# Optimization experiments

Measured on AMD Instinct MI355X. Metric: run time of the kernel, lower is better.

Reference implementation:

```python
import math
import jax, jax.numpy as jnp
import numpy as np

# Module hyperparameters (match init_kwargs)
EMBED = 512
H = 8            # n_heads
D = EMBED // H   # head_dim = 64
P = 32           # poly_dim
M = 4            # num_prf_features
R = 1            # num_quadrature_nodes
B = 1
T = 1024
EPS = 1e-6
C_CONST = 2.0 + EPS
# Gauss-Laguerre nodes/weights (R=1 -> node=1, weight=1), scaled by 1/C as in __init__
_nodes_np, _weights_np = np.polynomial.laguerre.laggauss(R)
QUAD_NODES = (_nodes_np / C_CONST).astype(np.float32)   # [R]


def setup_inputs() -> dict:
    key = jax.random.key(0)
    ks = jax.random.split(key, 6)
    x = jax.random.normal(ks[0], (B, T, EMBED), dtype=jnp.float32)
    qkv_w = jax.random.normal(ks[1], (3 * EMBED, EMBED), dtype=jnp.float32) * 0.02
    qkv_b = jnp.zeros((3 * EMBED,), dtype=jnp.float32)
    out_w = jax.random.normal(ks[2], (EMBED, EMBED), dtype=jnp.float32) * 0.02
    out_b = jnp.zeros((EMBED,), dtype=jnp.float32)
    omega = jax.random.normal(ks[3], (R, H, D, M), dtype=jnp.float32)  # PRF projection buffer
    poly_proj = jax.random.normal(ks[4], (H, D, P), dtype=jnp.float32) / math.sqrt(D)
    return {"x": x, "qkv_w": qkv_w, "qkv_b": qkv_b, "out_w": out_w,
            "out_b": out_b, "omega": omega, "poly_proj": poly_proj}


def _l2_normalize(z):
    # F.normalize(p=2, dim=-1), default eps=1e-12
    n = jnp.linalg.norm(z, axis=-1, keepdims=True)
    return z / jnp.maximum(n, 1e-12)


def _prf_features(x_norm, omega):
    # x_norm: [B,H,T,D], omega: [R,H,D,M] -> [R,B,H,T,M]
    proj = jnp.einsum('bhtd,rhdm->rbhtm', x_norm, omega)
    s = jnp.asarray(QUAD_NODES, x_norm.dtype).reshape(R, 1, 1, 1, 1)
    sqrt_2s = jnp.sqrt(2.0 * jnp.maximum(s, 0.0))
    exp_arg = jnp.clip(proj * sqrt_2s - s, -20.0, 20.0)
    return jnp.exp(exp_arg) / math.sqrt(M)


def _poly_features(x_norm, poly_proj):
    # squared random projection: [B,H,T,D] x [H,D,P] -> [B,H,T,P], nonneg
    p = jnp.einsum('bhtd,hdp->bhtp', x_norm, poly_proj)
    return p * p


def reference(x, qkv_w, qkv_b, out_w, out_b, omega, poly_proj):
    Bx, Tx, Cx = x.shape
    qkv = x @ qkv_w.T + qkv_b                       # [B,T,3C]
    q, k, v = jnp.split(qkv, 3, axis=-1)
    def to_heads(z):
        return z.reshape(Bx, Tx, H, D).transpose(0, 2, 1, 3)  # [B,H,T,D]
    q, k, v = to_heads(q), to_heads(k), to_heads(v)

    def full_features(z):
        zn = _l2_normalize(z)
        poly = _poly_features(zn, poly_proj)        # [B,H,T,P]
        prf = _prf_features(zn, omega)              # [R,B,H,T,M]
        return jnp.einsum('bhtp,rbhtm->rbhtpm', poly, prf)

    q_outer = full_features(q)                      # [R,B,H,T,P,M]
    k_outer = full_features(k)

    kv = jnp.einsum('rbhtpm,bhtd->rbhtpmd', k_outer, v)  # huge outer product
    kv_cumsum = jnp.cumsum(kv, axis=3)              # causal prefix sums along T
    k_cumsum = jnp.cumsum(k_outer, axis=3)

    context = jnp.einsum('rbhtpm,rbhtpmd->bhtd', q_outer, kv_cumsum)
    norm = jnp.einsum('rbhtpm,rbhtpm->bht', q_outer, k_cumsum)
    norm = jnp.maximum(norm, 1e-6)
    out = context / norm[..., None]                 # [B,H,T,D]

    out = out.transpose(0, 2, 1, 3).reshape(Bx, Tx, Cx)
    return out @ out_w.T + out_b
```

## Files before the change

kernel.cpp:

```cpp
#include <hip/hip_runtime.h>

#define T_LEN 1024
#define EMB   512
#define NH    8
#define HD    64
#define PDIM  32
#define MDIM  4
#define FDIM  128
#define TC    64
#define NC    16

typedef __attribute__((ext_vector_type(8))) short bf16x8;
typedef __attribute__((ext_vector_type(4))) float f32x4;

__device__ __forceinline__ unsigned short f2bf(float f) {
    unsigned u = __float_as_uint(f);
    unsigned r = u + 0x7fffu + ((u >> 16) & 1u);
    return (unsigned short)(r >> 16);
}
__device__ __forceinline__ float bf2f(unsigned short h) {
    return __uint_as_float(((unsigned)h) << 16);
}
__device__ __forceinline__ void split4(float4 v, ushort4& h4, ushort4& l4) {
    h4.x = f2bf(v.x); l4.x = f2bf(v.x - bf2f(h4.x));
    h4.y = f2bf(v.y); l4.y = f2bf(v.y - bf2f(h4.y));
    h4.z = f2bf(v.z); l4.z = f2bf(v.z - bf2f(h4.z));
    h4.w = f2bf(v.w); l4.w = f2bf(v.w - bf2f(h4.w));
}
__device__ __forceinline__ f32x4 mm3(bf16x8 ah, bf16x8 al, bf16x8 bh, bf16x8 bl, f32x4 acc) {
    acc = __builtin_amdgcn_mfma_f32_16x16x32_bf16(ah, bh, acc, 0, 0, 0);
    acc = __builtin_amdgcn_mfma_f32_16x16x32_bf16(ah, bl, acc, 0, 0, 0);
    acc = __builtin_amdgcn_mfma_f32_16x16x32_bf16(al, bh, acc, 0, 0, 0);
    return acc;
}
#define LD8(TILE, ROW, KB) (*reinterpret_cast<const bf16x8*>(&TILE[ROW][KB]))

__global__ __launch_bounds__(256) void k_cvt(
    const float* __restrict__ X, const float* __restrict__ Wq,
    const float* __restrict__ Wo,
    unsigned short* __restrict__ Xhi, unsigned short* __restrict__ Xlo,
    unsigned short* __restrict__ Whi, unsigned short* __restrict__ Wlo,
    unsigned short* __restrict__ Ohi, unsigned short* __restrict__ Olo)
{
    int i = (blockIdx.x * 256 + threadIdx.x) * 4;
    const float* src; unsigned short *dh, *dl; int off;
    if (i < 524288)       { src = X;  dh = Xhi; dl = Xlo; off = i; }
    else if (i < 1310720) { src = Wq; dh = Whi; dl = Wlo; off = i - 524288; }
    else                  { src = Wo; dh = Ohi; dl = Olo; off = i - 1310720; }
    float4 v = *reinterpret_cast<const float4*>(&src[off]);
    ushort4 h4, l4; split4(v, h4, l4);
    *reinterpret_cast<ushort4*>(&dh[off]) = h4;
    *reinterpret_cast<ushort4*>(&dl[off]) = l4;
}

__global__ __launch_bounds__(256) void k_qkv_mfma(
    const unsigned short* __restrict__ Xhi, const unsigned short* __restrict__ Xlo,
    const unsigned short* __restrict__ Whi, const unsigned short* __restrict__ Wlo,
    const float* __restrict__ bias,
    const float* __restrict__ poly_proj, const float* __restrict__ omega,
    unsigned short* __restrict__ Vhi, unsigned short* __restrict__ Vlo,
    unsigned short* __restrict__ qfhi, unsigned short* __restrict__ qflo,
    unsigned short* __restrict__ kfhi, unsigned short* __restrict__ kflo)
{
    const int j0 = blockIdx.x * 64;
    const int t0 = blockIdx.y * 64;
    __shared__ __align__(16) unsigned short Ahi[64][80], Alo[64][80],
                                            Bhi[64][80], Blo[64][80];
    __shared__ float poly_s[64][33];
    __shared__ float prf_s[64][5];
    __shared__ float nrm2[2][64];
    const int tid = threadIdx.x, lane = tid & 63, wid = tid >> 6;
    const int wrow = (wid >> 1) * 32, wcol = (wid & 1) * 32;
    const int lr = lane & 15, lg = lane >> 4;
    f32x4 acc[2][2];
    #pragma unroll
    for (int i = 0; i < 2; ++i)
        #pragma unroll
        for (int j = 0; j < 2; ++j) acc[i][j] = (f32x4){0.f, 0.f, 0.f, 0.f};

    for (int k0 = 0; k0 < 512; k0 += 64) {
        #pragma unroll
        for (int l = 0; l < 2; ++l) {
            int ch = tid + l * 256;
            int row = ch >> 3, sg = (ch & 7) * 8;
            size_t ao = (size_t)(t0 + row) * 512 + k0 + sg;
            size_t bo = (size_t)(j0 + row) * 512 + k0 + sg;
            *reinterpret_cast<int4*>(&Ahi[row][sg]) = *reinterpret_cast<const int4*>(&Xhi[ao]);
            *reinterpret_cast<int4*>(&Alo[row][sg]) = *reinterpret_cast<const int4*>(&Xlo[ao]);
            *reinterpret_cast<int4*>(&Bhi[row][sg]) = *reinterpret_cast<const int4*>(&Whi[bo]);
            *reinterpret_cast<int4*>(&Blo[row][sg]) = *reinterpret_cast<const int4*>(&Wlo[bo]);
        }
        __syncthreads();
        #pragma unroll
        for (int kh = 0; kh < 2; ++kh) {
            const int kb = kh * 32 + lg * 8;
            bf16x8 ah0 = LD8(Ahi, wrow + lr, kb),      ah1 = LD8(Ahi, wrow + 16 + lr, kb);
            bf16x8 al0 = LD8(Alo, wrow + lr, kb),      al1 = LD8(Alo, wrow + 16 + lr, kb);
            bf16x8 bh0 = LD8(Bhi, wcol + lr, kb),      bh1 = LD8(Bhi, wcol + 16 + lr, kb);
            bf16x8 bl0 = LD8(Blo, wcol + lr, kb),      bl1 = LD8(Blo, wcol + 16 + lr, kb);
            acc[0][0] = mm3(ah0, al0, bh0, bl0, acc[0][0]);
            acc[0][1] = mm3(ah0, al0, bh1, bl1, acc[0][1]);
            acc[1][0] = mm3(ah1, al1, bh0, bl0, acc[1][0]);
            acc[1][1] = mm3(ah1, al1, bh1, bl1, acc[1][1]);
        }
        __syncthreads();
    }
    const int which = j0 >> 9;
    const int h = (j0 & 511) >> 6;

    if (which == 2) {
        #pragma unroll
        for (int i = 0; i < 2; ++i)
            #pragma unroll
            for (int j = 0; j < 2; ++j)
                #pragma unroll
                for (int r = 0; r < 4; ++r) {
                    int row = wrow + i * 16 + lg * 4 + r;
                    int col = wcol + j * 16 + lr;
                    float val = acc[i][j][r] + bias[j0 + col];
                    unsigned short hv = f2bf(val);
                    size_t vi = (size_t)(h * T_LEN + t0 + row) * HD + col;
                    Vhi[vi] = hv; Vlo[vi] = f2bf(val - bf2f(hv));
                }
        return;
    }

    #pragma unroll
    for (int i = 0; i < 2; ++i) {
        #pragma unroll
        for (int r = 0; r < 4; ++r) {
            int row = wrow + i * 16 + lg * 4 + r;
            float ss = 0.f;
            #pragma unroll
            for (int j = 0; j < 2; ++j) {
                int col = wcol + j * 16 + lr;
                float zv = acc[i][j][r] + bias[j0 + col];
                ss = fmaf(zv, zv, ss);
                unsigned short hv = f2bf(zv);
                Ahi[row][col] = hv;
                Alo[row][col] = f2bf(zv - bf2f(hv));
            }
            ss += __shfl_xor(ss, 1, 64);
            ss += __shfl_xor(ss, 2, 64);
            ss += __shfl_xor(ss, 4, 64);
            ss += __shfl_xor(ss, 8, 64);
            if (lr == 0) nrm2[wid & 1][row] = ss;
        }
    }
    {
        const float* P = poly_proj + (size_t)h * 64 * 32;
        int d = tid >> 2, p8 = (tid & 3) * 8;
        #pragma unroll
        for (int e = 0; e < 8; ++e) {
            float pv = P[d * 32 + p8 + e];
            unsigned short hv = f2bf(pv);
            Bhi[p8 + e][d] = hv;
            Blo[p8 + e][d] = f2bf(pv - bf2f(hv));
        }
        if (tid < 64) {
            const float* Om = omega + (size_t)h * 64 * 4;
            float4 om = *reinterpret_cast<const float4*>(&Om[tid * 4]);
            float oa[4] = {om.x, om.y, om.z, om.w};
            #pragma unroll
            for (int m = 0; m < 4; ++m) {
                unsigned short hv = f2bf(oa[m]);
                Bhi[32 + m][tid] = hv;
                Blo[32 + m][tid] = f2bf(oa[m] - bf2f(hv));
            }
        }
        for (int rr = tid; rr < 12 * 64; rr += 256) {
            int row = 36 + (rr >> 6), dd = rr & 63;
            Bhi[row][dd] = 0; Blo[row][dd] = 0;
        }
    }
    __syncthreads();
    const int mrow = wid * 16;
    f32x4 g[3];
    g[0] = g[1] = g[2] = (f32x4){0.f, 0.f, 0.f, 0.f};
    #pragma unroll
    for (int kh = 0; kh < 2; ++kh) {
        const int kb = kh * 32 + lg * 8;
        bf16x8 ah = LD8(Ahi, mrow + lr, kb), al = LD8(Alo, mrow + lr, kb);
        #pragma unroll
        for (int j = 0; j < 3; ++j) {
            bf16x8 bh = LD8(Bhi, j * 16 + lr, kb), bl = LD8(Blo, j * 16 + lr, kb);
            g[j] = mm3(ah, al, bh, bl, g[j]);
        }
    }
    const float S_NODE = (float)(1.0 / 2.000001);
    const float SQRT2S = sqrtf(2.0f * S_NODE);
    #pragma unroll
    for (int r = 0; r < 4; ++r) {
        int row = mrow + lg * 4 + r;
        float rn = 1.0f / fmaxf(sqrtf(nrm2[0][row] + nrm2[1][row]), 1e-12f);
        #pragma unroll
        for (int j = 0; j < 3; ++j) {
            float gv = g[j][r] * rn;
            if (j < 2) poly_s[row][j * 16 + lr] = gv * gv;
            else if (lr < 4) {
                float arg = fminf(fmaxf(fmaf(gv, SQRT2S, -S_NODE), -20.0f), 20.0f);
                prf_s[row][lr] = expf(arg) * 0.5f;
            }
        }
    }
    {
        int row = mrow + (lane >> 2), fq = lane & 3;
        float pr[8], pf[4];
        #pragma unroll
        for (int e = 0; e < 8; ++e) pr[e] = poly_s[row][fq * 8 + e];
        #pragma unroll
        for (int m = 0; m < 4; ++m) pf[m] = prf_s[row][m];
        int4 hi4[4], lo4[4];
        unsigned short* hp = reinterpret_cast<unsigned short*>(hi4);
        unsigned short* lp = reinterpret_cast<unsigned short*>(lo4);
        #pragma unroll
        for (int e = 0; e < 8; ++e)
            #pragma unroll
            for (int m = 0; m < 4; ++m) {
                float val = pr[e] * pf[m];
                unsigned short hv = f2bf(val);
                hp[e * 4 + m] = hv;
                lp[e * 4 + m] = f2bf(val - bf2f(hv));
            }
        unsigned short* dhi = (which == 0) ? qfhi : kfhi;
        unsigned short* dlo = (which == 0) ? qflo : kflo;
        size_t base = (size_t)(h * T_LEN + t0 + row) * FDIM + fq * 32;
        #pragma unroll
        for (int s = 0; s < 4; ++s) {
            *reinterpret_cast<int4*>(&dhi[base + s * 8]) = hi4[s];
            *reinterpret_cast<int4*>(&dlo[base + s * 8]) = lo4[s];
        }
    }
}

__global__ __launch_bounds__(256) void k_out_mfma(
    const unsigned short* __restrict__ AThi, const unsigned short* __restrict__ ATlo,
    const unsigned short* __restrict__ Ohi, const unsigned short* __restrict__ Olo,
    const float* __restrict__ bias, float* __restrict__ Y)
{
    const int j0 = blockIdx.x * 64;
    const int t0 = blockIdx.y * 64;
    __shared__ __align__(16) unsigned short Ahi[64][80], Alo[64][80],
                                            Bhi[64][80], Blo[64][80];
    const int tid = threadIdx.x, lane = tid & 63, wid = tid >> 6;
    const int wrow = (wid >> 1) * 32, wcol = (wid & 1) * 32;
    const int lr = lane & 15, lg = lane >> 4;
    f32x4 acc[2][2];
    #pragma unroll
    for (int i = 0; i < 2; ++i)
        #pragma unroll
        for (int j = 0; j < 2; ++j) acc[i][j] = (f32x4){0.f, 0.f, 0.f, 0.f};

    for (int k0 = 0; k0 < 512; k0 += 64) {
        #pragma unroll
        for (int l = 0; l < 2; ++l) {
            int ch = tid + l * 256;
            int row = ch >> 3, sg = (ch & 7) * 8;
            size_t ao = (size_t)(t0 + row) * 512 + k0 + sg;
            size_t bo = (size_t)(j0 + row) * 512 + k0 + sg;
            *reinterpret_cast<int4*>(&Ahi[row][sg]) = *reinterpret_cast<const int4*>(&AThi[ao]);
            *reinterpret_cast<int4*>(&Alo[row][sg]) = *reinterpret_cast<const int4*>(&ATlo[ao]);
            *reinterpret_cast<int4*>(&Bhi[row][sg]) = *reinterpret_cast<const int4*>(&Ohi[bo]);
            *reinterpret_cast<int4*>(&Blo[row][sg]) = *reinterpret_cast<const int4*>(&Olo[bo]);
        }
        __syncthreads();
        #pragma unroll
        for (int kh = 0; kh < 2; ++kh) {
            const int kb = kh * 32 + lg * 8;
            bf16x8 ah0 = LD8(Ahi, wrow + lr, kb),      ah1 = LD8(Ahi, wrow + 16 + lr, kb);
            bf16x8 al0 = LD8(Alo, wrow + lr, kb),      al1 = LD8(Alo, wrow + 16 + lr, kb);
            bf16x8 bh0 = LD8(Bhi, wcol + lr, kb),      bh1 = LD8(Bhi, wcol + 16 + lr, kb);
            bf16x8 bl0 = LD8(Blo, wcol + lr, kb),      bl1 = LD8(Blo, wcol + 16 + lr, kb);
            acc[0][0] = mm3(ah0, al0, bh0, bl0, acc[0][0]);
            acc[0][1] = mm3(ah0, al0, bh1, bl1, acc[0][1]);
            acc[1][0] = mm3(ah1, al1, bh0, bl0, acc[1][0]);
            acc[1][1] = mm3(ah1, al1, bh1, bl1, acc[1][1]);
        }
        __syncthreads();
    }
    #pragma unroll
    for (int i = 0; i < 2; ++i)
        #pragma unroll
        for (int j = 0; j < 2; ++j)
            #pragma unroll
            for (int r = 0; r < 4; ++r) {
                int row = wrow + i * 16 + lg * 4 + r;
                int col = wcol + j * 16 + lr;
                Y[(size_t)(t0 + row) * EMB + j0 + col] = acc[i][j][r] + bias[j0 + col];
            }
}

__global__ __launch_bounds__(256) void k_chunk_kv(
    const unsigned short* __restrict__ kfhi, const unsigned short* __restrict__ kflo,
    const unsigned short* __restrict__ Vhi, const unsigned short* __restrict__ Vlo,
    float* __restrict__ SchT, float* __restrict__ zch,
    unsigned short* __restrict__ Vthi, unsigned short* __restrict__ Vtlo)
{
    const int b = blockIdx.x;
    const int fh = b & 1, hc = b >> 1, h = hc >> 4, c = hc & 15;
    const int t0 = c * TC;
    const int tid = threadIdx.x, lane = tid & 63, wid = tid >> 6;
    const int wrow = (wid >> 1) * 32, wcol = (wid & 1) * 32;
    const int lr = lane & 15, lg = lane >> 4;
    __shared__ __align__(16) unsigned short Khi[64][80], Klo[64][80],
                                            Ghi[64][80], Glo[64][80];
    #pragma unroll
    for (int l = 0; l < 2; ++l) {
        int ch = tid + l * 256;
        int t = ch >> 3, f8 = (ch & 7) * 8;
        int tb = t >> 3, tl = t & 7, m = f8 >> 3;
        size_t ko = (size_t)((h << 10) + t0 + t) * FDIM + fh * 64 + f8;
        int4 hv = *reinterpret_cast<const int4*>(&kfhi[ko]);
        int4 lv = *reinterpret_cast<const int4*>(&kflo[ko]);
        const unsigned short* hp = reinterpret_cast<const unsigned short*>(&hv);
        const unsigned short* lp = reinterpret_cast<const unsigned short*>(&lv);
        int col = ((tb ^ m) << 3) + tl;
        #pragma unroll
        for (int j = 0; j < 8; ++j) {
            Khi[f8 + j][col] = hp[j];
            Klo[f8 + j][col] = lp[j];
        }
    }
    #pragma unroll
    for (int l = 0; l < 4; ++l) {
        int ch = tid + l * 256;
        int plane = ch >> 9, rem = ch & 511;
        int t = rem >> 3, d8 = (rem & 7) * 8;
        int tb = t >> 3, tl = t & 7;
        const unsigned short* src = plane ? Vlo : Vhi;
        int4 vv = *reinterpret_cast<const int4*>(&src[(size_t)((h << 10) + t0 + t) * HD + d8]);
        const unsigned short* vp = reinterpret_cast<const unsigned short*>(&vv);
        int col = ((tb ^ (d8 >> 3)) << 3) + tl;
        unsigned short (*dst)[80] = plane ? Glo : Ghi;
        #pragma unroll
        for (int j = 0; j < 8; ++j) dst[d8 + j][col] = vp[j];
    }
    __syncthreads();
    f32x4 acc[2][2];
    #pragma unroll
    for (int i = 0; i < 2; ++i)
        #pragma unroll
        for (int j = 0; j < 2; ++j) acc[i][j] = (f32x4){0.f, 0.f, 0.f, 0.f};
    #pragma unroll
    for (int kh = 0; kh < 2; ++kh) {
        const int kb = kh * 32 + lg * 8, cb = kb >> 3;
        const int f0r = wcol + lr, f1r = wcol + 16 + lr;
        const int c0 = ((cb ^ ((f0r >> 3) & 7)) << 3), c1 = ((cb ^ ((f1r >> 3) & 7)) << 3);
        bf16x8 bh0 = *reinterpret_cast<const bf16x8*>(&Khi[f0r][c0]);
        bf16x8 bl0 = *reinterpret_cast<const bf16x8*>(&Klo[f0r][c0]);
        bf16x8 bh1 = *reinterpret_cast<const bf16x8*>(&Khi[f1r][c1]);
        bf16x8 bl1 = *reinterpret_cast<const bf16x8*>(&Klo[f1r][c1]);
        #pragma unroll
        for (int di = 0; di < 2; ++di) {
            int dr = wrow + di * 16 + lr;
            int ca = ((cb ^ ((dr >> 3) & 7)) << 3);
            bf16x8 ah = *reinterpret_cast<const bf16x8*>(&Ghi[dr][ca]);
            bf16x8 al = *reinterpret_cast<const bf16x8*>(&Glo[dr][ca]);
            acc[di][0] = mm3(ah, al, bh0, bl0, acc[di][0]);
            acc[di][1] = mm3(ah, al, bh1, bl1, acc[di][1]);
        }
    }
    if (tid < 64) {
        float s = 0.f;
        const int g = (tid >> 3) & 7;
        #pragma unroll
        for (int cb2 = 0; cb2 < 8; ++cb2) {
            int base = ((cb2 ^ g) << 3);
            #pragma unroll
            for (int e = 0; e < 8; ++e)
                s += bf2f(Khi[tid][base + e]) + bf2f(Klo[tid][base + e]);
        }
        zch[(h * NC + c) * FDIM + fh * 64 + tid] = s;
    }
    if (fh == 0) {
        #pragma unroll
        for (int l = 0; l < 4; ++l) {
            int ch = tid + l * 256;
            int plane = ch >> 9, rem = ch & 511;
            int d = rem >> 3, m = rem & 7;
            int g = (d >> 3) & 7;
            const unsigned short (*src)[80] = plane ? Glo : Ghi;
            unsigned short* dst = plane ? Vtlo : Vthi;
            *reinterpret_cast<int4*>(&dst[(size_t)(h * HD + d) * T_LEN + t0 + ((m ^ g) << 3)]) =
                *reinterpret_cast<const int4*>(&src[d][m << 3]);
        }
    }
    float* S = SchT + (size_t)(h * NC + c) * FDIM * HD;
    #pragma unroll
    for (int di = 0; di < 2; ++di)
        #pragma unroll
        for (int fj = 0; fj < 2; ++fj)
            #pragma unroll
            for (int r = 0; r < 4; ++r) {
                int d = wrow + di * 16 + lg * 4 + r;
                int f = fh * 64 + wcol + fj * 16 + lr;
                S[d * FDIM + f] = acc[di][fj][r];
            }
}

__global__ __launch_bounds__(256) void k_prefix(
    const float* __restrict__ SchT, const float* __restrict__ zch,
    unsigned short* __restrict__ SThi, unsigned short* __restrict__ STlo,
    float* __restrict__ zpre)
{
    const int h = blockIdx.x >> 4;
    const int e = ((blockIdx.x & 15) << 9) + threadIdx.x * 2;
    const size_t base = (size_t)h * NC * FDIM * HD + e;
    float2 vals[NC];
    #pragma unroll
    for (int c = 0; c < NC; ++c)
        vals[c] = *reinterpret_cast<const float2*>(&SchT[base + (size_t)c * FDIM * HD]);
    float r0 = 0.f, r1 = 0.f;
    #pragma unroll
    for (int c = 0; c < NC; ++c) {
        unsigned short h0 = f2bf(r0), h1 = f2bf(r1);
        unsigned short l0 = f2bf(r0 - bf2f(h0)), l1 = f2bf(r1 - bf2f(h1));
        size_t wi = base + (size_t)c * FDIM * HD;
        *reinterpret_cast<unsigned*>(&SThi[wi]) = (unsigned)h0 | ((unsigned)h1 << 16);
        *reinterpret_cast<unsigned*>(&STlo[wi]) = (unsigned)l0 | ((unsigned)l1 << 16);
        r0 += vals[c].x; r1 += vals[c].y;
    }
    if ((blockIdx.x & 15) == 0 && threadIdx.x < FDIM) {
        const int zb = h * NC * FDIM + threadIdx.x;
        float zv[NC];
        #pragma unroll
        for (int c = 0; c < NC; ++c) zv[c] = zch[zb + c * FDIM];
        float zr = 0.0f;
        #pragma unroll
        for (int c = 0; c < NC; ++c) { zpre[zb + c * FDIM] = zr; zr += zv[c]; }
    }
}

__global__ __launch_bounds__(256) void k_attn_mfma(
    const unsigned short* __restrict__ qfhi, const unsigned short* __restrict__ qflo,
    const unsigned short* __restrict__ kfhi, const unsigned short* __restrict__ kflo,
    const unsigned short* __restrict__ SThi, const unsigned short* __restrict__ STlo,
    const unsigned short* __restrict__ Vthi, const unsigned short* __restrict__ Vtlo,
    const float* __restrict__ zpre,
    unsigned short* __restrict__ AThi, unsigned short* __restrict__ ATlo)
{
    const int b = blockIdx.x;
    const int h = b >> 5, c = (b >> 1) & 15, half = b & 1;
    const int tc0 = c * TC;
    const int tq0 = tc0 + half * 32;
    const int tid = threadIdx.x, lane = tid & 63, wid = tid >> 6;
    const int wrow = (wid >> 1) * 16, wcol = (wid & 1) * 32;
    const int lr = lane & 15, lg = lane >> 4;

    __shared__ __align__(16) unsigned short T0[32][80], T1[32][80];
    __shared__ __align__(16) unsigned short T2[64][80], T3[64][80];
    __shared__ __align__(16) unsigned short T4[64][80], T5[64][80];
    __shared__ unsigned short zhi[FDIM], zlo[FDIM];
    __shared__ float nrm_part[2][32], nrm[32];

    if (tid < FDIM) {
        float zv = zpre[(h * NC + c) * FDIM + tid];
        unsigned short zh = f2bf(zv);
        zhi[tid] = zh; zlo[tid] = f2bf(zv - bf2f(zh));
    }

    f32x4 accA[2], accC[2], accN;
    accA[0] = accA[1] = accC[0] = accC[1] = accN = (f32x4){0.f, 0.f, 0.f, 0.f};

    for (int f0 = 0; f0 < FDIM; f0 += 64) {
        {
            int row = tid >> 3, sg = (tid & 7) * 8;
            size_t qo = (size_t)(h * T_LEN + tq0 + row) * FDIM + f0 + sg;
            *reinterpret_cast<int4*>(&T0[row][sg]) = *reinterpret_cast<const int4*>(&qfhi[qo]);
            *reinterpret_cast<int4*>(&T1[row][sg]) = *reinterpret_cast<const int4*>(&qflo[qo]);
        }
        #pragma unroll
        for (int l = 0; l < 2; ++l) {
            int ch = tid + l * 256;
            int row = ch >> 3, sg = (ch & 7) * 8;
            size_t ko = (size_t)(h * T_LEN + tc0 + row) * FDIM + f0 + sg;
            *reinterpret_cast<int4*>(&T2[row][sg]) = *reinterpret_cast<const int4*>(&kfhi[ko]);
            *reinterpret_cast<int4*>(&T3[row][sg]) = *reinterpret_cast<const int4*>(&kflo[ko]);
        }
        #pragma unroll
        for (int l = 0; l < 2; ++l) {
            int ch = tid + l * 256;
            int row = ch >> 3, sg = (ch & 7) * 8;
            size_t so = (size_t)(h * NC + c) * FDIM * HD + (size_t)row * FDIM + f0 + sg;
            *reinterpret_cast<int4*>(&T4[row][sg]) = *reinterpret_cast<const int4*>(&SThi[so]);
            *reinterpret_cast<int4*>(&T5[row][sg]) = *reinterpret_cast<const int4*>(&STlo[so]);
        }
        __syncthreads();
        #pragma unroll
        for (int kh = 0; kh < 2; ++kh) {
            const int kb = kh * 32 + lg * 8;
            bf16x8 qh = LD8(T0, wrow + lr, kb), ql = LD8(T1, wrow + lr, kb);
            bf16x8 kh0 = LD8(T2, wcol + lr, kb),      kh1 = LD8(T2, wcol + 16 + lr, kb);
            bf16x8 kl0 = LD8(T3, wcol + lr, kb),      kl1 = LD8(T3, wcol + 16 + lr, kb);
            bf16x8 sh0 = LD8(T4, wcol + lr, kb),      sh1 = LD8(T4, wcol + 16 + lr, kb);
            bf16x8 sl0 = LD8(T5, wcol + lr, kb),      sl1 = LD8(T5, wcol + 16 + lr, kb);
            accA[0] = mm3(qh, ql, kh0, kl0, accA[0]);
            accA[1] = mm3(qh, ql, kh1, kl1, accA[1]);
            accC[0] = mm3(qh, ql, sh0, sl0, accC[0]);
            accC[1] = mm3(qh, ql, sh1, sl1, accC[1]);
            bf16x8 zh8, zl8;
            #pragma unroll
            for (int j = 0; j < 8; ++j) {
                zh8[j] = (short)zhi[f0 + kb + j];
                zl8[j] = (short)zlo[f0 + kb + j];
            }
            accN = mm3(qh, ql, zh8, zl8, accN);
        }
        __syncthreads();
    }

    #pragma unroll
    for (int r = 0; r < 4; ++r) {
        int rowl = wrow + lg * 4 + r;
        int rowc = half * 32 + rowl;
        float rs = 0.f;
        #pragma unroll
        for (int j = 0; j < 2; ++j) {
            int col = wcol + j * 16 + lr;
            float vA = (col <= rowc) ? accA[j][r] : 0.f;
            rs += vA;
            unsigned short hv = f2bf(vA);
            T0[rowl][col] = hv;
            T1[rowl][col] = f2bf(vA - bf2f(hv));
        }
        #pragma unroll
        for (int off = 1; off < 16; off <<= 1) rs += __shfl_xor(rs, off, 64);
        if (lr == 0) {
            if ((wid & 1) == 0) nrm_part[0][rowl] = rs + accN[r];
            else                nrm_part[1][rowl] = rs;
        }
    }
    #pragma unroll
    for (int l = 0; l < 4; ++l) {
        int ch = tid + l * 256;
        int plane = ch >> 9, rem = ch & 511;
        int row = rem >> 3, sg = (rem & 7) * 8;
        size_t vo = (size_t)(h * HD + row) * T_LEN + tc0 + sg;
        const unsigned short* src = plane ? Vtlo : Vthi;
        unsigned short (*dst)[80] = plane ? T3 : T2;
        *reinterpret_cast<int4*>(&dst[row][sg]) = *reinterpret_cast<const int4*>(&src[vo]);
    }
    __syncthreads();
    if (tid < 32) nrm[tid] = fmaxf(nrm_part[0][tid] + nrm_part[1][tid], 1e-6f);

    #pragma unroll
    for (int kh = 0; kh < 2; ++kh) {
        const int kb = kh * 32 + lg * 8;
        bf16x8 ah = LD8(T0, wrow + lr, kb), al = LD8(T1, wrow + lr, kb);
        bf16x8 vh0 = LD8(T2, wcol + lr, kb),      vh1 = LD8(T2, wcol + 16 + lr, kb);
        bf16x8 vl0 = LD8(T3, wcol + lr, kb),      vl1 = LD8(T3, wcol + 16 + lr, kb);
        accC[0] = mm3(ah, al, vh0, vl0, accC[0]);
        accC[1] = mm3(ah, al, vh1, vl1, accC[1]);
    }
    __syncthreads();

    #pragma unroll
    for (int j = 0; j < 2; ++j)
        #pragma unroll
        for (int r = 0; r < 4; ++r) {
            int rowl = wrow + lg * 4 + r;
            int col = wcol + j * 16 + lr;
            float o = accC[j][r] / nrm[rowl];
            unsigned short hv = f2bf(o);
            size_t oi = (size_t)(tq0 + rowl) * EMB + h * HD + col;
            AThi[oi] = hv; ATlo[oi] = f2bf(o - bf2f(hv));
        }
}

extern "C" void kernel_launch(void* const* d_in, const int* in_sizes, int n_in,
                              void* d_out, int out_size, void* d_ws, size_t ws_size,
                              hipStream_t stream) {
    const float* x         = (const float*)d_in[0];
    const float* qkv_w     = (const float*)d_in[1];
    const float* qkv_b     = (const float*)d_in[2];
    const float* out_w     = (const float*)d_in[3];
    const float* out_b     = (const float*)d_in[4];
    const float* omega     = (const float*)d_in[5];
    const float* poly_proj = (const float*)d_in[6];
    float* out = (float*)d_out;

    unsigned short* Xhi  = (unsigned short*)d_ws;
    unsigned short* Xlo  = Xhi + 524288;
    unsigned short* Whi  = Xlo + 524288;
    unsigned short* Wlo  = Whi + 786432;
    unsigned short* Ohi  = Wlo + 786432;
    unsigned short* Olo  = Ohi + 262144;
    unsigned short* Vhi  = Olo + 262144;
    unsigned short* Vlo  = Vhi + 524288;
    unsigned short* qfhi = Vlo + 524288;
    unsigned short* qflo = qfhi + 1048576;
    unsigned short* kfhi = qflo + 1048576;
    unsigned short* kflo = kfhi + 1048576;
    float* SchT = (float*)(kflo + 1048576);
    unsigned short* SThi = (unsigned short*)(SchT + 1048576);
    unsigned short* STlo = SThi + 1048576;
    float* zch  = (float*)(STlo + 1048576);
    float* zpre = zch + 16384;
    unsigned short* AThi = Xhi;
    unsigned short* ATlo = Xlo;
    unsigned short* Vthi = Whi;
    unsigned short* Vtlo = Whi + 524288;

    k_cvt<<<1536, 256, 0, stream>>>(x, qkv_w, out_w, Xhi, Xlo, Whi, Wlo, Ohi, Olo);
    k_qkv_mfma<<<dim3(24, 16), 256, 0, stream>>>(Xhi, Xlo, Whi, Wlo, qkv_b,
                                                 poly_proj, omega, Vhi, Vlo,
                                                 qfhi, qflo, kfhi, kflo);
    k_chunk_kv<<<256, 256, 0, stream>>>(kfhi, kflo, Vhi, Vlo, SchT, zch, Vthi, Vtlo);
    k_prefix<<<128, 256, 0, stream>>>(SchT, zch, SThi, STlo, zpre);
    k_attn_mfma<<<NH * NC * 2, 256, 0, stream>>>(qfhi, qflo, kfhi, kflo, SThi, STlo,
                                                 Vthi, Vtlo, zpre, AThi, ATlo);
    k_out_mfma<<<dim3(8, 16), 256, 0, stream>>>(AThi, ATlo, Ohi, Olo, out_b, out);
}
```

Baseline: 111.4 us.

## Load attention MFMA operands directly from global memory, drop LDS staging

```diff
diff --git a/kernel.cpp b/kernel.cpp
--- a/kernel.cpp
+++ b/kernel.cpp
@@ -34,6 +34,7 @@
     return acc;
 }
 #define LD8(TILE, ROW, KB) (*reinterpret_cast<const bf16x8*>(&TILE[ROW][KB]))
+#define LDG8(PTR, IDX) (*reinterpret_cast<const bf16x8*>(&(PTR)[IDX]))
 
 __global__ __launch_bounds__(256) void k_cvt(
     const float* __restrict__ X, const float* __restrict__ Wq,
@@ -401,7 +402,7 @@
 __global__ __launch_bounds__(256) void k_prefix(
     const float* __restrict__ SchT, const float* __restrict__ zch,
     unsigned short* __restrict__ SThi, unsigned short* __restrict__ STlo,
-    float* __restrict__ zpre)
+    unsigned short* __restrict__ zphi, unsigned short* __restrict__ zplo)
 {
     const int h = blockIdx.x >> 4;
     const int e = ((blockIdx.x & 15) << 9) + threadIdx.x * 2;
@@ -427,7 +428,12 @@
         for (int c = 0; c < NC; ++c) zv[c] = zch[zb + c * FDIM];
         float zr = 0.0f;
         #pragma unroll
-        for (int c = 0; c < NC; ++c) { zpre[zb + c * FDIM] = zr; zr += zv[c]; }
+        for (int c = 0; c < NC; ++c) {
+            unsigned short zh = f2bf(zr);
+            zphi[zb + c * FDIM] = zh;
+            zplo[zb + c * FDIM] = f2bf(zr - bf2f(zh));
+            zr += zv[c];
+        }
     }
 }
 
@@ -436,7 +442,7 @@
     const unsigned short* __restrict__ kfhi, const unsigned short* __restrict__ kflo,
     const unsigned short* __restrict__ SThi, const unsigned short* __restrict__ STlo,
     const unsigned short* __restrict__ Vthi, const unsigned short* __restrict__ Vtlo,
-    const float* __restrict__ zpre,
+    const unsigned short* __restrict__ zphi, const unsigned short* __restrict__ zplo,
     unsigned short* __restrict__ AThi, unsigned short* __restrict__ ATlo)
 {
     const int b = blockIdx.x;
@@ -448,65 +454,36 @@
     const int lr = lane & 15, lg = lane >> 4;
 
     __shared__ __align__(16) unsigned short T0[32][80], T1[32][80];
-    __shared__ __align__(16) unsigned short T2[64][80], T3[64][80];
-    __shared__ __align__(16) unsigned short T4[64][80], T5[64][80];
-    __shared__ unsigned short zhi[FDIM], zlo[FDIM];
     __shared__ float nrm_part[2][32], nrm[32];
-
-    if (tid < FDIM) {
-        float zv = zpre[(h * NC + c) * FDIM + tid];
-        unsigned short zh = f2bf(zv);
-        zhi[tid] = zh; zlo[tid] = f2bf(zv - bf2f(zh));
-    }
 
     f32x4 accA[2], accC[2], accN;
     accA[0] = accA[1] = accC[0] = accC[1] = accN = (f32x4){0.f, 0.f, 0.f, 0.f};
 
+    const size_t qrow  = (size_t)(h * T_LEN + tq0 + wrow + lr) * FDIM;
+    const size_t krow0 = (size_t)(h * T_LEN + tc0 + wcol + lr) * FDIM;
+    const size_t krow1 = (size_t)(h * T_LEN + tc0 + wcol + 16 + lr) * FDIM;
+    const size_t sbase = (size_t)(h * NC + c) * FDIM * HD;
+    const size_t srow0 = sbase + (size_t)(wcol + lr) * FDIM;
+    const size_t srow1 = sbase + (size_t)(wcol + 16 + lr) * FDIM;
+    const size_t zrow  = (size_t)(h * NC + c) * FDIM;
+
+    #pragma unroll
     for (int f0 = 0; f0 < FDIM; f0 += 64) {
-        {
-            int row = tid >> 3, sg = (tid & 7) * 8;
-            size_t qo = (size_t)(h * T_LEN + tq0 + row) * FDIM + f0 + sg;
-            *reinterpret_cast<int4*>(&T0[row][sg]) = *reinterpret_cast<const int4*>(&qfhi[qo]);
-            *reinterpret_cast<int4*>(&T1[row][sg]) = *reinterpret_cast<const int4*>(&qflo[qo]);
-        }
-        #pragma unroll
-        for (int l = 0; l < 2; ++l) {
-            int ch = tid + l * 256;
-            int row = ch >> 3, sg = (ch & 7) * 8;
-            size_t ko = (size_t)(h * T_LEN + tc0 + row) * FDIM + f0 + sg;
-            *reinterpret_cast<int4*>(&T2[row][sg]) = *reinterpret_cast<const int4*>(&kfhi[ko]);
-            *reinterpret_cast<int4*>(&T3[row][sg]) = *reinterpret_cast<const int4*>(&kflo[ko]);
-        }
-        #pragma unroll
-        for (int l = 0; l < 2; ++l) {
-            int ch = tid + l * 256;
-            int row = ch >> 3, sg = (ch & 7) * 8;
-            size_t so = (size_t)(h * NC + c) * FDIM * HD + (size_t)row * FDIM + f0 + sg;
-            *reinterpret_cast<int4*>(&T4[row][sg]) = *reinterpret_cast<const int4*>(&SThi[so]);
-            *reinterpret_cast<int4*>(&T5[row][sg]) = *reinterpret_cast<const int4*>(&STlo[so]);
-        }
-        __syncthreads();
         #pragma unroll
         for (int kh = 0; kh < 2; ++kh) {
-            const int kb = kh * 32 + lg * 8;
-            bf16x8 qh = LD8(T0, wrow + lr, kb), ql = LD8(T1, wrow + lr, kb);
-            bf16x8 kh0 = LD8(T2, wcol + lr, kb),      kh1 = LD8(T2, wcol + 16 + lr, kb);
-            bf16x8 kl0 = LD8(T3, wcol + lr, kb),      kl1 = LD8(T3, wcol + 16 + lr, kb);
-            bf16x8 sh0 = LD8(T4, wcol + lr, kb),      sh1 = LD8(T4, wcol + 16 + lr, kb);
-            bf16x8 sl0 = LD8(T5, wcol + lr, kb),      sl1 = LD8(T5, wcol + 16 + lr, kb);
+            const int kb = f0 + kh * 32 + lg * 8;
+            bf16x8 qh  = LDG8(qfhi, qrow + kb),  ql  = LDG8(qflo, qrow + kb);
+            bf16x8 kh0 = LDG8(kfhi, krow0 + kb), kl0 = LDG8(kflo, krow0 + kb);
+            bf16x8 kh1 = LDG8(kfhi, krow1 + kb), kl1 = LDG8(kflo, krow1 + kb);
+            bf16x8 sh0 = LDG8(SThi, srow0 + kb), sl0 = LDG8(STlo, srow0 + kb);
+            bf16x8 sh1 = LDG8(SThi, srow1 + kb), sl1 = LDG8(STlo, srow1 + kb);
+            bf16x8 zh8 = LDG8(zphi, zrow + kb),  zl8 = LDG8(zplo, zrow + kb);
             accA[0] = mm3(qh, ql, kh0, kl0, accA[0]);
             accA[1] = mm3(qh, ql, kh1, kl1, accA[1]);
             accC[0] = mm3(qh, ql, sh0, sl0, accC[0]);
             accC[1] = mm3(qh, ql, sh1, sl1, accC[1]);
-            bf16x8 zh8, zl8;
-            #pragma unroll
-            for (int j = 0; j < 8; ++j) {
-                zh8[j] = (short)zhi[f0 + kb + j];
-                zl8[j] = (short)zlo[f0 + kb + j];
-            }
-            accN = mm3(qh, ql, zh8, zl8, accN);
-        }
-        __syncthreads();
+            accN    = mm3(qh, ql, zh8, zl8, accN);
+        }
     }
 
     #pragma unroll
@@ -530,25 +507,17 @@
             else                nrm_part[1][rowl] = rs;
         }
     }
-    #pragma unroll
-    for (int l = 0; l < 4; ++l) {
-        int ch = tid + l * 256;
-        int plane = ch >> 9, rem = ch & 511;
-        int row = rem >> 3, sg = (rem & 7) * 8;
-        size_t vo = (size_t)(h * HD + row) * T_LEN + tc0 + sg;
-        const unsigned short* src = plane ? Vtlo : Vthi;
-        unsigned short (*dst)[80] = plane ? T3 : T2;
-        *reinterpret_cast<int4*>(&dst[row][sg]) = *reinterpret_cast<const int4*>(&src[vo]);
-    }
     __syncthreads();
     if (tid < 32) nrm[tid] = fmaxf(nrm_part[0][tid] + nrm_part[1][tid], 1e-6f);
 
+    const size_t vrow0 = (size_t)(h * HD + wcol + lr) * T_LEN + tc0;
+    const size_t vrow1 = (size_t)(h * HD + wcol + 16 + lr) * T_LEN + tc0;
     #pragma unroll
     for (int kh = 0; kh < 2; ++kh) {
         const int kb = kh * 32 + lg * 8;
         bf16x8 ah = LD8(T0, wrow + lr, kb), al = LD8(T1, wrow + lr, kb);
-        bf16x8 vh0 = LD8(T2, wcol + lr, kb),      vh1 = LD8(T2, wcol + 16 + lr, kb);
-        bf16x8 vl0 = LD8(T3, wcol + lr, kb),      vl1 = LD8(T3, wcol + 16 + lr, kb);
+        bf16x8 vh0 = LDG8(Vthi, vrow0 + kb), vl0 = LDG8(Vtlo, vrow0 + kb);
+        bf16x8 vh1 = LDG8(Vthi, vrow1 + kb), vl1 = LDG8(Vtlo, vrow1 + kb);
         accC[0] = mm3(ah, al, vh0, vl0, accC[0]);
         accC[1] = mm3(ah, al, vh1, vl1, accC[1]);
     }
@@ -595,7 +564,8 @@
     unsigned short* SThi = (unsigned short*)(SchT + 1048576);
     unsigned short* STlo = SThi + 1048576;
     float* zch  = (float*)(STlo + 1048576);
-    float* zpre = zch + 16384;
+    unsigned short* zphi = (unsigned short*)(zch + 16384);
+    unsigned short* zplo = zphi + 16384;
     unsigned short* AThi = Xhi;
     unsigned short* ATlo = Xlo;
     unsigned short* Vthi = Whi;
@@ -606,8 +576,8 @@
                                                  poly_proj, omega, Vhi, Vlo,
                                                  qfhi, qflo, kfhi, kflo);
     k_chunk_kv<<<256, 256, 0, stream>>>(kfhi, kflo, Vhi, Vlo, SchT, zch, Vthi, Vtlo);
-    k_prefix<<<128, 256, 0, stream>>>(SchT, zch, SThi, STlo, zpre);
+    k_prefix<<<128, 256, 0, stream>>>(SchT, zch, SThi, STlo, zphi, zplo);
     k_attn_mfma<<<NH * NC * 2, 256, 0, stream>>>(qfhi, qflo, kfhi, kflo, SThi, STlo,
-                                                 Vthi, Vtlo, zpre, AThi, ATlo);
+                                                 Vthi, Vtlo, zphi, zplo, AThi, ATlo);
     k_out_mfma<<<dim3(8, 16), 256, 0, stream>>>(AThi, ATlo, Ohi, Olo, out_b, out);
 }
```

New measurement: 114.3 us. 1.03x slower.

## Fold chunk prefix-sum kernel into attention kernel loads

Applied to the files above, without the earlier changes.

```diff
diff --git a/kernel.cpp b/kernel.cpp
--- a/kernel.cpp
+++ b/kernel.cpp
@@ -398,45 +398,11 @@
             }
 }
 
-__global__ __launch_bounds__(256) void k_prefix(
-    const float* __restrict__ SchT, const float* __restrict__ zch,
-    unsigned short* __restrict__ SThi, unsigned short* __restrict__ STlo,
-    float* __restrict__ zpre)
-{
-    const int h = blockIdx.x >> 4;
-    const int e = ((blockIdx.x & 15) << 9) + threadIdx.x * 2;
-    const size_t base = (size_t)h * NC * FDIM * HD + e;
-    float2 vals[NC];
-    #pragma unroll
-    for (int c = 0; c < NC; ++c)
-        vals[c] = *reinterpret_cast<const float2*>(&SchT[base + (size_t)c * FDIM * HD]);
-    float r0 = 0.f, r1 = 0.f;
-    #pragma unroll
-    for (int c = 0; c < NC; ++c) {
-        unsigned short h0 = f2bf(r0), h1 = f2bf(r1);
-        unsigned short l0 = f2bf(r0 - bf2f(h0)), l1 = f2bf(r1 - bf2f(h1));
-        size_t wi = base + (size_t)c * FDIM * HD;
-        *reinterpret_cast<unsigned*>(&SThi[wi]) = (unsigned)h0 | ((unsigned)h1 << 16);
-        *reinterpret_cast<unsigned*>(&STlo[wi]) = (unsigned)l0 | ((unsigned)l1 << 16);
-        r0 += vals[c].x; r1 += vals[c].y;
-    }
-    if ((blockIdx.x & 15) == 0 && threadIdx.x < FDIM) {
-        const int zb = h * NC * FDIM + threadIdx.x;
-        float zv[NC];
-        #pragma unroll
-        for (int c = 0; c < NC; ++c) zv[c] = zch[zb + c * FDIM];
-        float zr = 0.0f;
-        #pragma unroll
-        for (int c = 0; c < NC; ++c) { zpre[zb + c * FDIM] = zr; zr += zv[c]; }
-    }
-}
-
 __global__ __launch_bounds__(256) void k_attn_mfma(
     const unsigned short* __restrict__ qfhi, const unsigned short* __restrict__ qflo,
     const unsigned short* __restrict__ kfhi, const unsigned short* __restrict__ kflo,
-    const unsigned short* __restrict__ SThi, const unsigned short* __restrict__ STlo,
+    const float* __restrict__ SchT, const float* __restrict__ zch,
     const unsigned short* __restrict__ Vthi, const unsigned short* __restrict__ Vtlo,
-    const float* __restrict__ zpre,
     unsigned short* __restrict__ AThi, unsigned short* __restrict__ ATlo)
 {
     const int b = blockIdx.x;
@@ -454,7 +420,8 @@
     __shared__ float nrm_part[2][32], nrm[32];
 
     if (tid < FDIM) {
-        float zv = zpre[(h * NC + c) * FDIM + tid];
+        float zv = 0.f;
+        for (int cc = 0; cc < c; ++cc) zv += zch[(h * NC + cc) * FDIM + tid];
         unsigned short zh = f2bf(zv);
         zhi[tid] = zh; zlo[tid] = f2bf(zv - bf2f(zh));
     }
@@ -481,9 +448,23 @@
         for (int l = 0; l < 2; ++l) {
             int ch = tid + l * 256;
             int row = ch >> 3, sg = (ch & 7) * 8;
-            size_t so = (size_t)(h * NC + c) * FDIM * HD + (size_t)row * FDIM + f0 + sg;
-            *reinterpret_cast<int4*>(&T4[row][sg]) = *reinterpret_cast<const int4*>(&SThi[so]);
-            *reinterpret_cast<int4*>(&T5[row][sg]) = *reinterpret_cast<const int4*>(&STlo[so]);
+            const float* Sb = SchT + (size_t)(h * NC) * FDIM * HD
+                                   + (size_t)row * FDIM + f0 + sg;
+            float4 s0 = make_float4(0.f, 0.f, 0.f, 0.f);
+            float4 s1 = make_float4(0.f, 0.f, 0.f, 0.f);
+            for (int cc = 0; cc < c; ++cc) {
+                const float* p = Sb + (size_t)cc * FDIM * HD;
+                float4 a = *reinterpret_cast<const float4*>(p);
+                float4 d = *reinterpret_cast<const float4*>(p + 4);
+                s0.x += a.x; s0.y += a.y; s0.z += a.z; s0.w += a.w;
+                s1.x += d.x; s1.y += d.y; s1.z += d.z; s1.w += d.w;
+            }
+            ushort4 h0, l0, h1, l1;
+            split4(s0, h0, l0); split4(s1, h1, l1);
+            *reinterpret_cast<ushort4*>(&T4[row][sg])     = h0;
+            *reinterpret_cast<ushort4*>(&T4[row][sg + 4]) = h1;
+            *reinterpret_cast<ushort4*>(&T5[row][sg])     = l0;
+            *reinterpret_cast<ushort4*>(&T5[row][sg + 4]) = l1;
         }
         __syncthreads();
         #pragma unroll
@@ -592,10 +573,7 @@
     unsigned short* kfhi = qflo + 1048576;
     unsigned short* kflo = kfhi + 1048576;
     float* SchT = (float*)(kflo + 1048576);
-    unsigned short* SThi = (unsigned short*)(SchT + 1048576);
-    unsigned short* STlo = SThi + 1048576;
-    float* zch  = (float*)(STlo + 1048576);
-    float* zpre = zch + 16384;
+    float* zch  = SchT + 1048576 + 524288;
     unsigned short* AThi = Xhi;
     unsigned short* ATlo = Xlo;
     unsigned short* Vthi = Whi;
@@ -606,8 +584,7 @@
                                                  poly_proj, omega, Vhi, Vlo,
                                                  qfhi, qflo, kfhi, kflo);
     k_chunk_kv<<<256, 256, 0, stream>>>(kfhi, kflo, Vhi, Vlo, SchT, zch, Vthi, Vtlo);
-    k_prefix<<<128, 256, 0, stream>>>(SchT, zch, SThi, STlo, zpre);
-    k_attn_mfma<<<NH * NC * 2, 256, 0, stream>>>(qfhi, qflo, kfhi, kflo, SThi, STlo,
-                                                 Vthi, Vtlo, zpre, AThi, ATlo);
+    k_attn_mfma<<<NH * NC * 2, 256, 0, stream>>>(qfhi, qflo, kfhi, kflo, SchT, zch,
+                                                 Vthi, Vtlo, AThi, ATlo);
     k_out_mfma<<<dim3(8, 16), 256, 0, stream>>>(AThi, ATlo, Ohi, Olo, out_b, out);
 }
```

After: 121.4 us. 1.09x slower.
